# Kernel tuning notes

Measured on AMD Instinct MI355X. Metric: run time of the kernel, lower is better.

Reference implementation:

```python
import jax, jax.numpy as jnp
import numpy as np

NUM_GROUPS = 32
EPS = 1e-6


def group_norm(x, weight, bias):
    # x: [b, c, h, w]
    b, c, h, w = x.shape
    xg = x.reshape(b, NUM_GROUPS, c // NUM_GROUPS, h, w)
    mean = jnp.mean(xg, axis=(2, 3, 4), keepdims=True)
    var = jnp.var(xg, axis=(2, 3, 4), keepdims=True)
    xn = ((xg - mean) * jax.lax.rsqrt(var + EPS)).reshape(b, c, h, w)
    return xn * weight[None, :, None, None] + bias[None, :, None, None]


def conv1x1(x, w, b):
    # 1x1 conv == per-pixel matmul. x: [b, c_in, h, w], w: [c_out, c_in]
    return jnp.einsum('oi,bihw->bohw', w, x) + b[None, :, None, None]


def setup_inputs() -> dict:
    key = jax.random.key(0)
    ks = jax.random.split(key, 9)
    b, c, h, w = 8, 512, 64, 64
    scale = 1.0 / np.sqrt(c)
    return {
        'x': jax.random.normal(ks[0], (b, c, h, w), jnp.float32),
        'gn_weight': jnp.ones((c,), jnp.float32),
        'gn_bias': jnp.zeros((c,), jnp.float32),
        'wq': jax.random.normal(ks[1], (c, c), jnp.float32) * scale,
        'bq': jnp.zeros((c,), jnp.float32),
        'wk': jax.random.normal(ks[2], (c, c), jnp.float32) * scale,
        'bk': jnp.zeros((c,), jnp.float32),
        'wv': jax.random.normal(ks[3], (c, c), jnp.float32) * scale,
        'bv': jnp.zeros((c,), jnp.float32),
        'wp': jax.random.normal(ks[4], (c, c), jnp.float32) * scale,
        'bp': jnp.zeros((c,), jnp.float32),
    }


def reference(x, gn_weight, gn_bias, wq, bq, wk, bk, wv, bv, wp, bp):
    h_ = group_norm(x, gn_weight, gn_bias)
    q = conv1x1(h_, wq, bq)
    k = conv1x1(h_, wk, bk)
    v = conv1x1(h_, wv, bv)
    b, c, h, w = q.shape
    n = h * w
    qf = q.reshape(b, c, n)
    kf = k.reshape(b, c, n)
    vf = v.reshape(b, c, n)
    # scores: [b, q, k]
    scores = jnp.einsum('bcq,bck->bqk', qf, kf) * (c ** -0.5)
    attn = jax.nn.softmax(scores, axis=-1)
    out = jnp.einsum('bqk,bck->bcq', attn, vf).reshape(b, c, h, w)
    out = conv1x1(out, wp, bp)
    return x + out
```

## Files before the change

### kernel.cpp

```cpp
#include <hip/hip_runtime.h>
#include <cstdint>

typedef unsigned short u16;
typedef __bf16 bf16x8 __attribute__((ext_vector_type(8)));
typedef float f32x4 __attribute__((ext_vector_type(4)));

__device__ __forceinline__ u16 f2bf(float f) {
    uint32_t u = __float_as_uint(f);
    u += 0x7FFFu + ((u >> 16) & 1u);
    return (u16)(u >> 16);
}
__device__ __forceinline__ float bf2f(u16 v) {
    return __uint_as_float((uint32_t)v << 16);
}

__device__ __forceinline__ void gload16(const u16* g, u16* l) {
    __builtin_amdgcn_global_load_lds(
        (const __attribute__((address_space(1))) uint32_t*)g,
        (__attribute__((address_space(3))) uint32_t*)l, 16, 0, 0);
}

__device__ __forceinline__ void swz(int& n_idx, int& m_idx, int& z_idx) {
    const int nx = gridDim.x, ny = gridDim.y;
    int lid = blockIdx.x + nx * (blockIdx.y + ny * blockIdx.z);
    int g = lid & 7, h = lid >> 3;
    n_idx = h % nx;
    int pair = (h / nx) * 8 + g;
    m_idx = pair % ny;
    z_idx = pair / ny;
}

__global__ __launch_bounds__(256) void k_detect(const u16* __restrict__ x,
                                                int* __restrict__ flag) {
    const int t = threadIdx.x;
    uint32_t mx = 0;
    for (int i = 0; i < 256; i++) {
        uint32_t v = (uint32_t)x[i * 256 + t] & 0x7FFFu;
        mx = mx > v ? mx : v;
    }
    for (int off = 32; off > 0; off >>= 1) {
        uint32_t o = (uint32_t)__shfl_xor((int)mx, off);
        mx = mx > o ? mx : o;
    }
    __shared__ uint32_t r[4];
    if ((t & 63) == 0) r[t >> 6] = mx;
    __syncthreads();
    if (t == 0) {
        uint32_t a = r[0] > r[1] ? r[0] : r[1];
        uint32_t b = r[2] > r[3] ? r[2] : r[3];
        mx = a > b ? a : b;
        *flag = (mx > 0x5000u) ? 1 : 0;
    }
}

__global__ __launch_bounds__(256) void k_cvt_wb(const void* wq, const void* wk,
                                                const void* wv, const void* wp,
                                                const void* gw, const void* gb,
                                                const void* bq, const void* bk,
                                                const void* bv, const void* bp,
                                                const int* __restrict__ flag,
                                                u16* __restrict__ Wc,
                                                u16* __restrict__ Bc) {
    const int mode = *flag;
    int i = blockIdx.x * 256 + threadIdx.x;
    if (i >= 1048576 + 3072) return;
    const void* src;
    u16* dst;
    int off;
    if (i < 1048576) {
        int which = i >> 18;
        off = i & 262143;
        src = which == 0 ? wq : which == 1 ? wk : which == 2 ? wv : wp;
        dst = Wc + i;
    } else {
        int j = i - 1048576;
        int which = j >> 9;
        off = j & 511;
        src = which == 0 ? gw : which == 1 ? gb : which == 2 ? bq
            : which == 3 ? bk : which == 4 ? bv : bp;
        dst = Bc + j;
    }
    *dst = mode ? f2bf(((const float*)src)[off]) : ((const u16*)src)[off];
}

__global__ __launch_bounds__(256) void k_gn_stats(const void* __restrict__ x_raw,
                                                  const u16* __restrict__ Bc,
                                                  const int* __restrict__ flag,
                                                  float* __restrict__ Sc,
                                                  float* __restrict__ Sh) {
    const int b = blockIdx.x >> 5, g = blockIdx.x & 31;
    const int mode = *flag;
    const int t = threadIdx.x;
    const int wave = t >> 6, lane = t & 63;
    float s = 0.f, ss = 0.f;
    if (mode) {
        const float4* xb = (const float4*)((const float*)x_raw +
                                           ((size_t)b * 512 + g * 16) * 4096);
        for (int it = 0; it < 64; it++) {
            float4 v = xb[it * 256 + t];
            s += v.x + v.y + v.z + v.w;
            ss += v.x * v.x + v.y * v.y + v.z * v.z + v.w * v.w;
        }
    } else {
        const uint4* xb = (const uint4*)((const u16*)x_raw +
                                         ((size_t)b * 512 + g * 16) * 4096);
        for (int it = 0; it < 32; it++) {
            uint4 v = xb[it * 256 + t];
            uint32_t w[4] = {v.x, v.y, v.z, v.w};
            for (int j = 0; j < 4; j++) {
                float a = __uint_as_float(w[j] << 16);
                float c = __uint_as_float(w[j] & 0xFFFF0000u);
                s += a + c;
                ss += a * a + c * c;
            }
        }
    }
    for (int off = 32; off > 0; off >>= 1) {
        s += __shfl_xor(s, off);
        ss += __shfl_xor(ss, off);
    }
    __shared__ float rs[4], rss[4];
    if (lane == 0) { rs[wave] = s; rss[wave] = ss; }
    __syncthreads();
    s = rs[0] + rs[1] + rs[2] + rs[3];
    ss = rss[0] + rss[1] + rss[2] + rss[3];
    const float mean = s * (1.f / 65536.f);
    const float var = ss * (1.f / 65536.f) - mean * mean;
    const float rstd = rsqrtf(var + 1e-6f);
    if (t < 16) {
        int c = g * 16 + t;
        float w = bf2f(Bc[c]);
        Sc[b * 512 + c] = rstd * w;
        Sh[b * 512 + c] = bf2f(Bc[512 + c]) - mean * rstd * w;
    }
}

#define TPAD 520
__global__ __launch_bounds__(256) void k_gn_apply(const void* __restrict__ x_raw,
                                                  const int* __restrict__ flag,
                                                  const float* __restrict__ Sc,
                                                  const float* __restrict__ Sh,
                                                  u16* __restrict__ HT) {
    __shared__ u16 tile[64 * TPAD];
    __shared__ float sSc[512], sSh[512];
    const int b = blockIdx.y;
    const int p0 = blockIdx.x * 64;
    const int mode = *flag;
    const int t = threadIdx.x;
    sSc[t] = Sc[b * 512 + t]; sSc[t + 256] = Sc[b * 512 + t + 256];
    sSh[t] = Sh[b * 512 + t]; sSh[t + 256] = Sh[b * 512 + t + 256];
    __syncthreads();
    for (int it = 0; it < 16; it++) {
        int li = it * 256 + t;
        int c = li >> 3;
        int pj = (li & 7) * 8;
        float v[8];
        if (mode) {
            const float* xr = (const float*)x_raw + ((size_t)b * 512 + c) * 4096 + p0 + pj;
            float4 a = *(const float4*)xr;
            float4 d = *(const float4*)(xr + 4);
            v[0] = a.x; v[1] = a.y; v[2] = a.z; v[3] = a.w;
            v[4] = d.x; v[5] = d.y; v[6] = d.z; v[7] = d.w;
        } else {
            const u16* xr = (const u16*)x_raw + ((size_t)b * 512 + c) * 4096 + p0 + pj;
            uint4 a = *(const uint4*)xr;
            uint32_t w[4] = {a.x, a.y, a.z, a.w};
            for (int j = 0; j < 4; j++) {
                v[2 * j] = __uint_as_float(w[j] << 16);
                v[2 * j + 1] = __uint_as_float(w[j] & 0xFFFF0000u);
            }
        }
        float sc = sSc[c], sh = sSh[c];
        for (int k = 0; k < 8; k++)
            tile[(pj + k) * TPAD + c] = f2bf(v[k] * sc + sh);
    }
    __syncthreads();
    u16* H = HT + (size_t)b * 2097152 + (size_t)p0 * 512;
    for (int it = 0; it < 16; it++) {
        int ch = it * 256 + t;
        int pp = ch >> 6;
        int cc = (ch & 63) * 8;
        *(uint4*)&H[(size_t)pp * 512 + cc] = *(const uint4*)&tile[pp * TPAD + cc];
    }
}

__device__ __forceinline__ void gemm_core(const u16* __restrict__ A,
                                          const u16* __restrict__ BT,
                                          int lda, int ldb, int K,
                                          int m0, int n0,
                                          u16* lA, u16* lB,
                                          f32x4 (&acc)[4][4]) {
    const int t = threadIdx.x;
    const int wave = t >> 6, lane = t & 63;
    const int wm = (wave >> 1) * 64, wn = (wave & 1) * 64;
    const int mf = lane & 15, quad = lane >> 4;
    const int srow = t >> 3;
    const int scol = (((t & 7) ^ (srow & 7)) * 8);
    const u16* Ap = A + (size_t)(m0 + srow) * lda + scol;
    const u16* Bp = BT + (size_t)(n0 + srow) * ldb + scol;
    u16* lAd = &lA[t * 8];
    u16* lBd = &lB[t * 8];
    const int fx = mf & 7;

    for (int i = 0; i < 4; i++)
        for (int j = 0; j < 4; j++)
            acc[i][j] = (f32x4){0.f, 0.f, 0.f, 0.f};

    for (int k0 = 0; k0 < K; k0 += 64) {
        __syncthreads();
        gload16(Ap + k0, lAd);
        gload16(Ap + k0 + (size_t)32 * lda, lAd + 2048);
        gload16(Ap + k0 + (size_t)64 * lda, lAd + 4096);
        gload16(Ap + k0 + (size_t)96 * lda, lAd + 6144);
        gload16(Bp + k0, lBd);
        gload16(Bp + k0 + (size_t)32 * ldb, lBd + 2048);
        gload16(Bp + k0 + (size_t)64 * ldb, lBd + 4096);
        gload16(Bp + k0 + (size_t)96 * ldb, lBd + 6144);
        __syncthreads();
        for (int ks = 0; ks < 2; ks++) {
            bf16x8 af[4], bfr[4];
            const int sl = ((ks * 4 + quad) ^ fx) * 8;
            for (int i = 0; i < 4; i++)
                af[i] = *(const bf16x8*)&lA[(wm + i * 16 + mf) * 64 + sl];
            for (int j = 0; j < 4; j++)
                bfr[j] = *(const bf16x8*)&lB[(wn + j * 16 + mf) * 64 + sl];
            for (int i = 0; i < 4; i++)
                for (int j = 0; j < 4; j++)
                    acc[i][j] = __builtin_amdgcn_mfma_f32_16x16x32_bf16(af[i], bfr[j], acc[i][j], 0, 0, 0);
        }
    }
}

__global__ __launch_bounds__(256) void k_qkv(const u16* __restrict__ HT,
                                             const u16* __restrict__ Wc,
                                             const u16* __restrict__ Bc,
                                             u16* __restrict__ QT,
                                             u16* __restrict__ KT,
                                             u16* __restrict__ V) {
    __shared__ __align__(16) u16 sm[16384];
    int nI, mI, zI;
    swz(nI, mI, zI);
    const int b = zI / 3, s = zI % 3;
    const u16* Bb = Bc + 1024 + s * 512;
    int m0, n0, ldo, bias_by_row;
    const u16 *A, *BT;
    u16* O;
    if (s < 2) {
        m0 = mI * 128; n0 = nI * 128;
        A = HT + (size_t)b * 2097152; BT = Wc + (size_t)s * 262144;
        O = (s == 0 ? QT : KT) + (size_t)b * 2097152; ldo = 512; bias_by_row = 0;
    } else {
        m0 = nI * 128; n0 = mI * 128;
        A = Wc + (size_t)2 * 262144; BT = HT + (size_t)b * 2097152;
        O = V + (size_t)b * 2097152; ldo = 4096; bias_by_row = 1;
    }
    f32x4 acc[4][4];
    gemm_core(A, BT, 512, 512, 512, m0, n0, sm, sm + 8192, acc);

    const int t = threadIdx.x;
    const int wave = t >> 6, lane = t & 63;
    const int wm = (wave >> 1) * 64, wn = (wave & 1) * 64;
    const int mf = lane & 15, quad = lane >> 4;
    __syncthreads();
    for (int i = 0; i < 4; i++)
        for (int r = 0; r < 4; r++) {
            int row = wm + i * 16 + quad * 4 + r;
            int kk = ((row >> 2) & 3) << 4;
            for (int j = 0; j < 4; j++) {
                int col = wn + j * 16 + mf;
                float bias = bf2f(Bb[bias_by_row ? (m0 + row) : (n0 + col)]);
                sm[row * 128 + (col ^ kk)] = f2bf(acc[i][j][r] + bias);
            }
        }
    __syncthreads();
    for (int p = 0; p < 8; p++) {
        int idx = p * 256 + t;
        int rowt = idx >> 4, c8 = (idx & 15) * 8;
        int kk = ((rowt >> 2) & 3) << 4;
        uint4 v = *(const uint4*)&sm[rowt * 128 + (c8 ^ kk)];
        *(uint4*)&O[(size_t)(m0 + rowt) * ldo + n0 + c8] = v;
    }
}

__device__ __forceinline__ u16* s_ptr(u16* S_ht, u16* S_tail, int l) {
    return l == 0 ? S_ht : S_tail + (size_t)(l - 1) * 16777216;
}

__global__ __launch_bounds__(512, 2) void k_scores(const u16* __restrict__ QT,
                                                   const u16* __restrict__ KT,
                                                   u16* __restrict__ S_ht,
                                                   u16* __restrict__ S_tail,
                                                   float* __restrict__ Part,
                                                   int b0) {
    __shared__ __align__(16) u16 lds[65536];
    int nI, mI, l;
    swz(nI, mI, l);
    const int n0 = nI * 256;
    const int m0 = mI * 256;
    const int b = b0 + l;
    const u16* Aq = QT + (size_t)b * 2097152;
    const u16* Bk = KT + (size_t)b * 2097152;

    const int t = threadIdx.x;
    const int wave = t >> 6, lane = t & 63;
    const int wm = (wave >> 2) * 128, wn = (wave & 3) * 64;
    const int mf = lane & 15, quad = lane >> 4;
    const int fx = mf & 7;
    const int srow = t >> 3;
    const int scol8 = t & 7;

    f32x4 acc[8][4];
#pragma unroll
    for (int i = 0; i < 8; i++)
#pragma unroll
        for (int j = 0; j < 4; j++)
            acc[i][j] = (f32x4){0.f, 0.f, 0.f, 0.f};

    auto issueA = [&](u16* dst, int h, int k0) {
#pragma unroll
        for (int s = 0; s < 2; s++) {
            int row = h * 128 + s * 64 + srow;
            gload16(Aq + (size_t)(m0 + row) * 512 + k0 + ((scol8 ^ (row & 7)) << 3),
                    dst + h * 8192 + s * 4096 + t * 8);
        }
    };
    auto issueB = [&](u16* dst, int h, int k0) {
#pragma unroll
        for (int s = 0; s < 2; s++) {
            int row = h * 128 + s * 64 + srow;
            gload16(Bk + (size_t)(n0 + row) * 512 + k0 + ((scol8 ^ (row & 7)) << 3),
                    dst + h * 8192 + s * 4096 + t * 8);
        }
    };

    issueA(lds, 0, 0); issueA(lds, 1, 0);
    issueB(lds + 16384, 0, 0); issueB(lds + 16384, 1, 0);

    for (int kt = 0; kt < 8; kt++) {
        u16* lA = (kt & 1) ? lds + 32768 : lds;
        u16* lB = lA + 16384;
        u16* pA = (kt & 1) ? lds : lds + 32768;
        u16* pB = pA + 16384;
        const int k0n = (kt + 1) << 6;
        const bool pf = kt < 7;
        asm volatile("" ::: "memory");
        __builtin_amdgcn_s_barrier();
        asm volatile("" ::: "memory");
        if (pf) {
            issueA(pA, 0, k0n);
            asm volatile("s_waitcnt vmcnt(2)" ::: "memory");
        } else {
            asm volatile("s_waitcnt vmcnt(0)" ::: "memory");
        }
        __builtin_amdgcn_s_barrier();
        asm volatile("" ::: "memory");

        bf16x8 af[8], bfr[2];
        int sl = (quad ^ fx) * 8;
#pragma unroll
        for (int i = 0; i < 8; i++)
            af[i] = *(const bf16x8*)&lA[(wm + i * 16 + mf) * 64 + sl];
#pragma unroll
        for (int j = 0; j < 2; j++)
            bfr[j] = *(const bf16x8*)&lB[(wn + j * 16 + mf) * 64 + sl];
        __builtin_amdgcn_s_setprio(1);
#pragma unroll
        for (int i = 0; i < 8; i++)
#pragma unroll
            for (int j = 0; j < 2; j++)
                acc[i][j] = __builtin_amdgcn_mfma_f32_16x16x32_bf16(af[i], bfr[j], acc[i][j], 0, 0, 0);
        __builtin_amdgcn_s_setprio(0);
        if (pf) issueA(pA, 1, k0n);
#pragma unroll
        for (int j = 0; j < 2; j++)
            bfr[j] = *(const bf16x8*)&lB[(wn + (2 + j) * 16 + mf) * 64 + sl];
        __builtin_amdgcn_s_setprio(1);
#pragma unroll
        for (int i = 0; i < 8; i++)
#pragma unroll
            for (int j = 0; j < 2; j++)
                acc[i][2 + j] = __builtin_amdgcn_mfma_f32_16x16x32_bf16(af[i], bfr[j], acc[i][2 + j], 0, 0, 0);
        __builtin_amdgcn_s_setprio(0);
        sl = ((4 + quad) ^ fx) * 8;
        if (pf) issueB(pB, 0, k0n);
#pragma unroll
        for (int i = 0; i < 8; i++)
            af[i] = *(const bf16x8*)&lA[(wm + i * 16 + mf) * 64 + sl];
#pragma unroll
        for (int j = 0; j < 2; j++)
            bfr[j] = *(const bf16x8*)&lB[(wn + j * 16 + mf) * 64 + sl];
        __builtin_amdgcn_s_setprio(1);
#pragma unroll
        for (int i = 0; i < 8; i++)
#pragma unroll
            for (int j = 0; j < 2; j++)
                acc[i][j] = __builtin_amdgcn_mfma_f32_16x16x32_bf16(af[i], bfr[j], acc[i][j], 0, 0, 0);
        __builtin_amdgcn_s_setprio(0);
        if (pf) issueB(pB, 1, k0n);
#pragma unroll
        for (int j = 0; j < 2; j++)
            bfr[j] = *(const bf16x8*)&lB[(wn + (2 + j) * 16 + mf) * 64 + sl];
        __builtin_amdgcn_s_setprio(1);
#pragma unroll
        for (int i = 0; i < 8; i++)
#pragma unroll
            for (int j = 0; j < 2; j++)
                acc[i][2 + j] = __builtin_amdgcn_mfma_f32_16x16x32_bf16(af[i], bfr[j], acc[i][2 + j], 0, 0, 0);
        __builtin_amdgcn_s_setprio(0);
    }

    const float scale = 0.04419417382415922f;
    __syncthreads();
#pragma unroll
    for (int i = 0; i < 8; i++)
#pragma unroll
        for (int r = 0; r < 4; r++) {
            int row = wm + i * 16 + quad * 4 + r;
            int key = row & 7;
#pragma unroll
            for (int j = 0; j < 4; j++) {
                int col = wn + j * 16 + mf;
                lds[row * 256 + (((col >> 3) ^ key) << 3) + (col & 7)] =
                    f2bf(__expf(acc[i][j][r] * scale));
            }
        }
    __syncthreads();
    u16* Sb = s_ptr(S_ht, S_tail, l);
    float* pr = Part + ((size_t)b * 16 + nI) * 4096 + m0;
    for (int p = 0; p < 16; p++) {
        int idx = p * 512 + t;
        int row = idx >> 5, chunk = idx & 31;
        uint4 v = *(const uint4*)&lds[row * 256 + ((chunk ^ (row & 7)) << 3)];
        uint32_t w[4] = {v.x, v.y, v.z, v.w};
        float s = 0.f;
        for (int q2 = 0; q2 < 4; q2++)
            s += __uint_as_float(w[q2] << 16) + __uint_as_float(w[q2] & 0xFFFF0000u);
        for (int off = 16; off > 0; off >>= 1) s += __shfl_xor(s, off);
        if ((lane & 31) == 0) pr[row] = s;
        *(uint4*)&Sb[(size_t)(m0 + row) * 4096 + n0 + chunk * 8] = v;
    }
}

__global__ __launch_bounds__(256) void k_pv_split(u16* __restrict__ S_ht,
                                                  u16* __restrict__ S_tail,
                                                  const u16* __restrict__ V,
                                                  u16* __restrict__ QT,
                                                  u16* __restrict__ KT,
                                                  int b0) {
    __shared__ __align__(16) u16 sm[16384];
    int nI, mI, zI;
    swz(nI, mI, zI);
    const int n0 = nI * 128;
    const int m0 = mI * 128;
    const int l = zI >> 1, split = zI & 1, b = b0 + l;
    const u16* A = s_ptr(S_ht, S_tail, l) + split * 2048;
    const u16* BT = V + (size_t)b * 2097152 + split * 2048;
    f32x4 acc[4][4];
    gemm_core(A, BT, 4096, 4096, 2048, m0, n0, sm, sm + 8192, acc);

    const int t = threadIdx.x;
    const int wave = t >> 6, lane = t & 63;
    const int wm = (wave >> 1) * 64, wn = (wave & 1) * 64;
    const int mf = lane & 15, quad = lane >> 4;
    u16* P = (split == 0 ? QT : KT) + (size_t)b * 2097152;
    __syncthreads();
    for (int i = 0; i < 4; i++)
        for (int r = 0; r < 4; r++) {
            int row = wm + i * 16 + quad * 4 + r;
            int kk = ((row >> 2) & 3) << 4;
            for (int j = 0; j < 4; j++) {
                int col = wn + j * 16 + mf;
                sm[row * 128 + (col ^ kk)] = f2bf(acc[i][j][r]);
            }
        }
    __syncthreads();
    for (int p = 0; p < 8; p++) {
        int idx = p * 256 + t;
        int rowt = idx >> 4, c8 = (idx & 15) * 8;
        int kk = ((rowt >> 2) & 3) << 4;
        uint4 v = *(const uint4*)&sm[rowt * 128 + (c8 ^ kk)];
        *(uint4*)&P[(size_t)(m0 + rowt) * 512 + n0 + c8] = v;
    }
}

__global__ __launch_bounds__(256) void k_pv_reduce(const u16* __restrict__ QT,
                                                   const u16* __restrict__ KT,
                                                   const float* __restrict__ Part,
                                                   u16* __restrict__ OT,
                                                   int b0) {
    const int b = b0 + blockIdx.y;
    const int t = threadIdx.x;
    __shared__ float sInv[4];
    if (t < 64) {
        int r = t >> 4, which = t & 15;
        int p = blockIdx.x * 4 + r;
        float v = Part[((size_t)b * 16 + which) * 4096 + p];
        for (int off = 8; off > 0; off >>= 1) v += __shfl_xor(v, off);
        if (which == 0) sInv[r] = 1.f / v;
    }
    __syncthreads();
    const float inv = sInv[t >> 6];
    size_t base = (size_t)b * 2097152;
    size_t i0 = base + ((size_t)blockIdx.x * 256 + t) * 8;
    uint4 a = *(const uint4*)(QT + i0);
    uint4 c = *(const uint4*)(KT + i0);
    uint32_t wa[4] = {a.x, a.y, a.z, a.w};
    uint32_t wc[4] = {c.x, c.y, c.z, c.w};
    uint32_t o[4];
    for (int j = 0; j < 4; j++) {
        float lo = (__uint_as_float(wa[j] << 16) + __uint_as_float(wc[j] << 16)) * inv;
        float hi = (__uint_as_float(wa[j] & 0xFFFF0000u) + __uint_as_float(wc[j] & 0xFFFF0000u)) * inv;
        o[j] = (uint32_t)f2bf(lo) | ((uint32_t)f2bf(hi) << 16);
    }
    *(uint4*)(OT + i0) = make_uint4(o[0], o[1], o[2], o[3]);
}

__global__ __launch_bounds__(256) void k_proj(const u16* __restrict__ Wc,
                                              const u16* __restrict__ OT,
                                              const u16* __restrict__ Bc,
                                              const void* __restrict__ x_raw,
                                              const int* __restrict__ flag,
                                              void* __restrict__ y_raw) {
    __shared__ __align__(16) u16 smu[16384];
    float* smf = (float*)smu;
    int nI, mI, b;
    swz(nI, mI, b);
    const int n0 = nI * 128;
    const int m0 = mI * 128;
    f32x4 acc[4][4];
    gemm_core(Wc + (size_t)3 * 262144, OT + (size_t)b * 2097152, 512, 512, 512,
              m0, n0, smu, smu + 8192, acc);

    const int mode = *flag;
    const u16* bp = Bc + 5 * 512;
    const int t = threadIdx.x;
    const int wave = t >> 6, lane = t & 63;
    const int wn = (wave & 1) * 64;
    const int mf = lane & 15, quad = lane >> 4;
    const int whalf = wave >> 1;
    size_t bb = (size_t)b * 2097152;
    for (int h = 0; h < 2; h++) {
        __syncthreads();
        if (whalf == h) {
            for (int i = 0; i < 4; i++)
                for (int r = 0; r < 4; r++) {
                    int rowl = i * 16 + quad * 4 + r;
                    int kf = ((rowl >> 2) & 1) << 4;
                    for (int j = 0; j < 4; j++) {
                        int col = wn + j * 16 + mf;
                        smf[rowl * 128 + (col ^ kf)] = acc[i][j][r];
                    }
                }
        }
        __syncthreads();
        const int rowbase = m0 + h * 64;
        if (mode) {
            for (int p = 0; p < 8; p++) {
                int idx = p * 256 + t;
                int rowl = idx >> 5, c4 = (idx & 31) * 4;
                int kf = ((rowl >> 2) & 1) << 4;
                f32x4 v = *(const f32x4*)&smf[rowl * 128 + (c4 ^ kf)];
                int rowg = rowbase + rowl;
                float bias = bf2f(bp[rowg]);
                size_t o = bb + (size_t)rowg * 4096 + n0 + c4;
                float4 xv = *(const float4*)((const float*)x_raw + o);
                float4 out = make_float4(v[0] + bias + xv.x, v[1] + bias + xv.y,
                                         v[2] + bias + xv.z, v[3] + bias + xv.w);
                *(float4*)((float*)y_raw + o) = out;
            }
        } else {
            for (int p = 0; p < 4; p++) {
                int idx = p * 256 + t;
                int rowl = idx >> 4, c8 = (idx & 15) * 8;
                int kf = ((rowl >> 2) & 1) << 4;
                const float* sp = &smf[rowl * 128 + (c8 ^ kf)];
                f32x4 v0 = *(const f32x4*)sp;
                f32x4 v1 = *(const f32x4*)(sp + 4);
                int rowg = rowbase + rowl;
                float bias = bf2f(bp[rowg]);
                size_t o = bb + (size_t)rowg * 4096 + n0 + c8;
                uint4 xv = *(const uint4*)((const u16*)x_raw + o);
                uint32_t xw[4] = {xv.x, xv.y, xv.z, xv.w};
                float vals[8] = {v0[0], v0[1], v0[2], v0[3],
                                 v1[0], v1[1], v1[2], v1[3]};
                uint32_t ow[4];
                for (int q2 = 0; q2 < 4; q2++) {
                    float lo = __uint_as_float(xw[q2] << 16) + vals[2 * q2] + bias;
                    float hi = __uint_as_float(xw[q2] & 0xFFFF0000u) + vals[2 * q2 + 1] + bias;
                    ow[q2] = (uint32_t)f2bf(lo) | ((uint32_t)f2bf(hi) << 16);
                }
                *(uint4*)((u16*)y_raw + o) = make_uint4(ow[0], ow[1], ow[2], ow[3]);
            }
        }
    }
}

extern "C" void kernel_launch(void* const* d_in, const int* in_sizes, int n_in,
                              void* d_out, int out_size, void* d_ws, size_t ws_size,
                              hipStream_t stream) {
    (void)in_sizes; (void)n_in; (void)out_size;
    const void* x  = d_in[0];
    const void* gw = d_in[1];
    const void* gb = d_in[2];
    const void* wq = d_in[3];
    const void* bq = d_in[4];
    const void* wk = d_in[5];
    const void* bk = d_in[6];
    const void* wv = d_in[7];
    const void* bv = d_in[8];
    const void* wp = d_in[9];
    const void* bp = d_in[10];

    u16* ws16 = (u16*)d_ws;
    int* flag = (int*)d_ws;
    float* Sc = (float*)(ws16 + 16);
    float* Sh = Sc + 4096;
    u16* Wc = ws16 + 16 + 16384;
    u16* Bc = Wc + 1048576;
    u16* HT = Bc + 4096;
    u16* QT = HT + 16777216;
    u16* KT = QT + 16777216;
    u16* V  = KT + 16777216;
    u16* OT = V  + 16777216;
    float* Part = (float*)(OT + 16777216);
    u16* Tail = (u16*)(Part + 1048576);
    const size_t base_elems = (size_t)(Tail - ws16);

    int nb = 1;
    for (int cand = 8; cand >= 2; cand >>= 1) {
        size_t need = 2ull * (base_elems + (size_t)(cand - 1) * 16777216ull);
        if (ws_size >= need) { nb = cand; break; }
    }

    k_detect<<<1, 256, 0, stream>>>((const u16*)x, flag);
    k_cvt_wb<<<4108, 256, 0, stream>>>(wq, wk, wv, wp, gw, gb, bq, bk, bv, bp,
                                       flag, Wc, Bc);
    k_gn_stats<<<256, 256, 0, stream>>>(x, Bc, flag, Sc, Sh);
    k_gn_apply<<<dim3(64, 8), 256, 0, stream>>>(x, flag, Sc, Sh, HT);
    k_qkv<<<dim3(4, 32, 24), 256, 0, stream>>>(HT, Wc, Bc, QT, KT, V);
    for (int b0 = 0; b0 < 8; b0 += nb) {
        k_scores<<<dim3(16, 16, nb), 512, 0, stream>>>(QT, KT, HT, Tail, Part, b0);
        k_pv_split<<<dim3(4, 32, 2 * nb), 256, 0, stream>>>(HT, Tail, V, QT, KT, b0);
        k_pv_reduce<<<dim3(1024, nb), 256, 0, stream>>>(QT, KT, Part, OT, b0);
    }
    k_proj<<<dim3(32, 4, 8), 256, 0, stream>>>(Wc, OT, Bc, x, flag, d_out);
}
```

Measured before the change: 722.4 us.

## Widen PV split GEMM tile to 128x256 with pipelined 512-thread main loop

Replaces the generic gemm_core call in the PV split kernel with a custom 128x256 tile, 8-wave mainloop that double-buffers A and B in LDS, interleaves async global-to-LDS loads between MFMA groups, and raises wave priority around MFMAs. The larger N tile halves the grid along N and improves reuse of the A (scores) tile, cutting global traffic for S. It uses more LDS (96 KB) and registers per block, which may limit occupancy, and the epilogue is rewritten with a new XOR swizzle for 256-wide rows.

```diff
diff --git a/kernel.cpp b/kernel.cpp
--- a/kernel.cpp
+++ b/kernel.cpp
@@ -441,45 +441,150 @@
     }
 }
 
-__global__ __launch_bounds__(256) void k_pv_split(u16* __restrict__ S_ht,
-                                                  u16* __restrict__ S_tail,
-                                                  const u16* __restrict__ V,
-                                                  u16* __restrict__ QT,
-                                                  u16* __restrict__ KT,
-                                                  int b0) {
-    __shared__ __align__(16) u16 sm[16384];
+__global__ __launch_bounds__(512, 2) void k_pv_split(u16* __restrict__ S_ht,
+                                                     u16* __restrict__ S_tail,
+                                                     const u16* __restrict__ V,
+                                                     u16* __restrict__ QT,
+                                                     u16* __restrict__ KT,
+                                                     int b0) {
+    __shared__ __align__(16) u16 lds[49152];
     int nI, mI, zI;
     swz(nI, mI, zI);
-    const int n0 = nI * 128;
+    const int n0 = nI * 256;
     const int m0 = mI * 128;
     const int l = zI >> 1, split = zI & 1, b = b0 + l;
     const u16* A = s_ptr(S_ht, S_tail, l) + split * 2048;
-    const u16* BT = V + (size_t)b * 2097152 + split * 2048;
+    const u16* B = V + (size_t)b * 2097152 + split * 2048;
+
+    const int t = threadIdx.x;
+    const int wave = t >> 6, lane = t & 63;
+    const int wm = (wave >> 2) * 64, wn = (wave & 3) * 64;
+    const int mf = lane & 15, quad = lane >> 4;
+    const int fx = mf & 7;
+    const int srow = t >> 3;
+    const int scol8 = t & 7;
+
     f32x4 acc[4][4];
-    gemm_core(A, BT, 4096, 4096, 2048, m0, n0, sm, sm + 8192, acc);
-
-    const int t = threadIdx.x;
-    const int wave = t >> 6, lane = t & 63;
-    const int wm = (wave >> 1) * 64, wn = (wave & 1) * 64;
-    const int mf = lane & 15, quad = lane >> 4;
+#pragma unroll
+    for (int i = 0; i < 4; i++)
+#pragma unroll
+        for (int j = 0; j < 4; j++)
+            acc[i][j] = (f32x4){0.f, 0.f, 0.f, 0.f};
+
+    auto issueA = [&](u16* dst, int k0) {
+#pragma unroll
+        for (int s = 0; s < 2; s++) {
+            int row = s * 64 + srow;
+            gload16(A + (size_t)(m0 + row) * 4096 + k0 + ((scol8 ^ (row & 7)) << 3),
+                    dst + s * 4096 + t * 8);
+        }
+    };
+    auto issueB = [&](u16* dst, int h, int k0) {
+#pragma unroll
+        for (int s = 0; s < 2; s++) {
+            int row = h * 128 + s * 64 + srow;
+            gload16(B + (size_t)(n0 + row) * 4096 + k0 + ((scol8 ^ (row & 7)) << 3),
+                    dst + h * 8192 + s * 4096 + t * 8);
+        }
+    };
+
+    issueA(lds, 0);
+    issueB(lds + 8192, 0, 0);
+    issueB(lds + 8192, 1, 0);
+
+    for (int kt = 0; kt < 32; kt++) {
+        u16* lA = (kt & 1) ? lds + 24576 : lds;
+        u16* lB = lA + 8192;
+        u16* pA = (kt & 1) ? lds : lds + 24576;
+        u16* pB = pA + 8192;
+        const int k0n = (kt + 1) << 6;
+        const bool pf = kt < 31;
+        asm volatile("" ::: "memory");
+        __builtin_amdgcn_s_barrier();
+        asm volatile("" ::: "memory");
+        if (pf) {
+            issueA(pA, k0n);
+            asm volatile("s_waitcnt vmcnt(2)" ::: "memory");
+        } else {
+            asm volatile("s_waitcnt vmcnt(0)" ::: "memory");
+        }
+        __builtin_amdgcn_s_barrier();
+        asm volatile("" ::: "memory");
+
+        bf16x8 af[4], bfr[2];
+        int sl = (quad ^ fx) * 8;
+#pragma unroll
+        for (int i = 0; i < 4; i++)
+            af[i] = *(const bf16x8*)&lA[(wm + i * 16 + mf) * 64 + sl];
+#pragma unroll
+        for (int j = 0; j < 2; j++)
+            bfr[j] = *(const bf16x8*)&lB[(wn + j * 16 + mf) * 64 + sl];
+        __builtin_amdgcn_s_setprio(1);
+#pragma unroll
+        for (int i = 0; i < 4; i++)
+#pragma unroll
+            for (int j = 0; j < 2; j++)
+                acc[i][j] = __builtin_amdgcn_mfma_f32_16x16x32_bf16(af[i], bfr[j], acc[i][j], 0, 0, 0);
+        __builtin_amdgcn_s_setprio(0);
+        if (pf) issueB(pB, 0, k0n);
+#pragma unroll
+        for (int j = 0; j < 2; j++)
+            bfr[j] = *(const bf16x8*)&lB[(wn + (2 + j) * 16 + mf) * 64 + sl];
+        __builtin_amdgcn_s_setprio(1);
+#pragma unroll
+        for (int i = 0; i < 4; i++)
+#pragma unroll
+            for (int j = 0; j < 2; j++)
+                acc[i][2 + j] = __builtin_amdgcn_mfma_f32_16x16x32_bf16(af[i], bfr[j], acc[i][2 + j], 0, 0, 0);
+        __builtin_amdgcn_s_setprio(0);
+        sl = ((4 + quad) ^ fx) * 8;
+        if (pf) issueB(pB, 1, k0n);
+#pragma unroll
+        for (int i = 0; i < 4; i++)
+            af[i] = *(const bf16x8*)&lA[(wm + i * 16 + mf) * 64 + sl];
+#pragma unroll
+        for (int j = 0; j < 2; j++)
+            bfr[j] = *(const bf16x8*)&lB[(wn + j * 16 + mf) * 64 + sl];
+        __builtin_amdgcn_s_setprio(1);
+#pragma unroll
+        for (int i = 0; i < 4; i++)
+#pragma unroll
+            for (int j = 0; j < 2; j++)
+                acc[i][j] = __builtin_amdgcn_mfma_f32_16x16x32_bf16(af[i], bfr[j], acc[i][j], 0, 0, 0);
+        __builtin_amdgcn_s_setprio(0);
+#pragma unroll
+        for (int j = 0; j < 2; j++)
+            bfr[j] = *(const bf16x8*)&lB[(wn + (2 + j) * 16 + mf) * 64 + sl];
+        __builtin_amdgcn_s_setprio(1);
+#pragma unroll
+        for (int i = 0; i < 4; i++)
+#pragma unroll
+            for (int j = 0; j < 2; j++)
+                acc[i][2 + j] = __builtin_amdgcn_mfma_f32_16x16x32_bf16(af[i], bfr[j], acc[i][2 + j], 0, 0, 0);
+        __builtin_amdgcn_s_setprio(0);
+    }
+
     u16* P = (split == 0 ? QT : KT) + (size_t)b * 2097152;
     __syncthreads();
+#pragma unroll
     for (int i = 0; i < 4; i++)
+#pragma unroll
         for (int r = 0; r < 4; r++) {
             int row = wm + i * 16 + quad * 4 + r;
-            int kk = ((row >> 2) & 3) << 4;
+            int key = row & 7;
+#pragma unroll
             for (int j = 0; j < 4; j++) {
                 int col = wn + j * 16 + mf;
-                sm[row * 128 + (col ^ kk)] = f2bf(acc[i][j][r]);
+                lds[row * 256 + (((col >> 3) ^ key) << 3) + (col & 7)] =
+                    f2bf(acc[i][j][r]);
             }
         }
     __syncthreads();
     for (int p = 0; p < 8; p++) {
-        int idx = p * 256 + t;
-        int rowt = idx >> 4, c8 = (idx & 15) * 8;
-        int kk = ((rowt >> 2) & 3) << 4;
-        uint4 v = *(const uint4*)&sm[rowt * 128 + (c8 ^ kk)];
-        *(uint4*)&P[(size_t)(m0 + rowt) * 512 + n0 + c8] = v;
+        int idx = p * 512 + t;
+        int row = idx >> 5, chunk = idx & 31;
+        uint4 v = *(const uint4*)&lds[row * 256 + ((chunk ^ (row & 7)) << 3)];
+        *(uint4*)&P[(size_t)(m0 + row) * 512 + n0 + chunk * 8] = v;
     }
 }
 
@@ -640,7 +745,7 @@
     k_qkv<<<dim3(4, 32, 24), 256, 0, stream>>>(HT, Wc, Bc, QT, KT, V);
     for (int b0 = 0; b0 < 8; b0 += nb) {
         k_scores<<<dim3(16, 16, nb), 512, 0, stream>>>(QT, KT, HT, Tail, Part, b0);
-        k_pv_split<<<dim3(4, 32, 2 * nb), 256, 0, stream>>>(HT, Tail, V, QT, KT, b0);
+        k_pv_split<<<dim3(2, 32, 2 * nb), 512, 0, stream>>>(HT, Tail, V, QT, KT, b0);
         k_pv_reduce<<<dim3(1024, nb), 256, 0, stream>>>(QT, KT, Part, OT, b0);
     }
     k_proj<<<dim3(32, 4, 8), 256, 0, stream>>>(Wc, OT, Bc, x, flag, d_out);
```

Result: faster. 701.0 us (-3.0%).
